# Optimization experiments

Hardware: AMD Instinct MI355X
Metric: run time of the kernel (lower is better)

## Reference

```python
import jax, jax.numpy as jnp
import numpy as np

N_EMBD = 1024
N_HEAD = 16
HEAD_DIM = N_EMBD // N_HEAD
B, T = 8, 1024


def setup_inputs() -> dict:
    key = jax.random.key(0)
    k1, k2, k3, k4 = jax.random.split(key, 4)
    x = jax.random.normal(k1, (B, T, N_EMBD), dtype=jnp.float32)
    # nn.Linear weight shapes: qkv (3C, C) no bias; proj (C, C) with bias
    w_qkv = jax.random.normal(k2, (3 * N_EMBD, N_EMBD), dtype=jnp.float32) * 0.02
    w_proj = jax.random.normal(k3, (N_EMBD, N_EMBD), dtype=jnp.float32) * 0.02
    b_proj = jax.random.normal(k4, (N_EMBD,), dtype=jnp.float32) * 0.02
    return {"x": x, "w_qkv": w_qkv, "w_proj": w_proj, "b_proj": b_proj}


def reference(x, w_qkv, w_proj, b_proj):
    Bq, Tq, C = x.shape
    qkv = jnp.einsum('btc,dc->btd', x, w_qkv)  # (B,T,3C)
    q, k, v = jnp.split(qkv, 3, axis=-1)
    def heads(t):
        return t.reshape(Bq, Tq, N_HEAD, HEAD_DIM).transpose(0, 2, 1, 3)  # (B,H,T,D)
    q, k, v = heads(q), heads(k), heads(v)
    scale = 1.0 / np.sqrt(HEAD_DIM).astype(np.float32)
    att = jnp.einsum('bhqd,bhkd->bhqk', q, k) * scale  # (B,H,T,T)
    causal = jnp.tril(jnp.ones((Tq, Tq), dtype=bool))
    att = jnp.where(causal, att, -jnp.inf)
    att = jax.nn.softmax(att, axis=-1)
    # dropout: eval mode -> identity
    y = jnp.einsum('bhqk,bhkd->bhqd', att, v)
    y = y.transpose(0, 2, 1, 3).reshape(Bq, Tq, C)
    return jnp.einsum('btc,dc->btd', y, w_proj) + b_proj
```

## Files before the change

### kernel.cpp

```cpp
#include <hip/hip_runtime.h>
#include <stdint.h>


#define Bn 8
#define Tn 1024
#define Cn 1024
#define Hn 16
#define Dn 64
#define Mn (Bn * Tn)
#define NQKV (3 * Cn)
#define QKS 2048

typedef unsigned short u16;
typedef float f32x4 __attribute__((ext_vector_type(4)));
typedef __bf16 bf16x8 __attribute__((ext_vector_type(8)));
typedef unsigned short ushx8 __attribute__((ext_vector_type(8)));
typedef unsigned short ushx4 __attribute__((ext_vector_type(4)));

__device__ __forceinline__ u16 f2bf(float f) {
  unsigned int u = __float_as_uint(f);
  u += 0x7fffu + ((u >> 16) & 1u);
  return (u16)(u >> 16);
}
__device__ __forceinline__ u16 f2bf_rna(float f) {
  return (u16)((__float_as_uint(f) + 0x8000u) >> 16);
}

__device__ __forceinline__ f32x4 mfma_bf16(ushx8 a, ushx8 b, f32x4 c) {
  return __builtin_amdgcn_mfma_f32_16x16x32_bf16(
      __builtin_bit_cast(bf16x8, a), __builtin_bit_cast(bf16x8, b), c, 0, 0, 0);
}

__device__ __forceinline__ void async16(const u16* g, u16* l) {
  __builtin_amdgcn_global_load_lds(
      (__attribute__((address_space(1))) void*)(void*)g,
      (__attribute__((address_space(3))) void*)l, 16, 0, 0);
}

template <int CTRL>
__device__ __forceinline__ float dppmov(float v) {
  return __builtin_bit_cast(float, __builtin_amdgcn_update_dpp(
      0, __builtin_bit_cast(int, v), CTRL, 0xf, 0xf, true));
}
__device__ __forceinline__ float red16max(float v) {
  v = fmaxf(v, dppmov<0xB1>(v));
  v = fmaxf(v, dppmov<0x4E>(v));
  v = fmaxf(v, dppmov<0x141>(v));
  v = fmaxf(v, dppmov<0x140>(v));
  return v;
}
__device__ __forceinline__ float red16sum(float v) {
  v += dppmov<0xB1>(v);
  v += dppmov<0x4E>(v);
  v += dppmov<0x141>(v);
  v += dppmov<0x140>(v);
  return v;
}

__global__ void cast3_kernel(const float* __restrict__ a, u16* __restrict__ oa, int na4,
                             const float* __restrict__ b, u16* __restrict__ ob, int nb4,
                             const float* __restrict__ c, u16* __restrict__ oc, int nc4) {
  int i = blockIdx.x * blockDim.x + threadIdx.x;
  const float* in;
  u16* out;
  if (i < na4) { in = a; out = oa; }
  else if (i < na4 + nb4) { in = b; out = ob; i -= na4; }
  else if (i < na4 + nb4 + nc4) { in = c; out = oc; i -= na4 + nb4; }
  else return;
  float4 v = ((const float4*)in)[i];
  ushx4 o = { f2bf(v.x), f2bf(v.y), f2bf(v.z), f2bf(v.w) };
  ((ushx4*)out)[i] = o;
}

#define SLOG2E 0.18033688011112042f
template <int QKV>
__global__ __launch_bounds__(256, 4) void gemm_bt(
    const u16* __restrict__ A, const u16* __restrict__ Bw,
    void* __restrict__ Cout, u16* __restrict__ vt,
    const float* __restrict__ bias, int N, int K) {
  __shared__ alignas(16) u16 As[128 * 32];
  __shared__ alignas(16) u16 Bs[128 * 32];

  const int tid = threadIdx.x;
  const int lane = tid & 63;
  const int wv = tid >> 6;
  const int quad = lane >> 4;
  const int l16 = lane & 15;
  const int m0 = blockIdx.x * 128;
  const int n0 = blockIdx.y * 128;
  const int wm = (wv >> 1) * 64;
  const int wn = (wv & 1) * 64;

  f32x4 acc[4][4];
#pragma unroll
  for (int i = 0; i < 4; ++i)
#pragma unroll
    for (int j = 0; j < 4; ++j) acc[i][j] = (f32x4){0.f, 0.f, 0.f, 0.f};

  const int r0 = tid >> 2;
  const int cc0 = tid & 3;
  const int gkc0 = cc0 ^ ((r0 >> 1) & 3);
  const int r1 = r0 + 64;
  const int gkc1 = cc0 ^ ((r1 >> 1) & 3);
  const u16* gA0 = A + (size_t)(m0 + r0) * K + gkc0 * 8;
  const u16* gA1 = A + (size_t)(m0 + r1) * K + gkc1 * 8;
  const u16* gB0 = Bw + (size_t)(n0 + r0) * K + gkc0 * 8;
  const u16* gB1 = Bw + (size_t)(n0 + r1) * K + gkc1 * 8;
  u16* lA0 = As + tid * 8;
  u16* lA1 = As + (256 + tid) * 8;
  u16* lB0 = Bs + tid * 8;
  u16* lB1 = Bs + (256 + tid) * 8;

  const u16* pa[4];
  const u16* pb[4];
#pragma unroll
  for (int mi = 0; mi < 4; ++mi) {
    int ra = wm + mi * 16 + l16;
    pa[mi] = As + ra * 32 + (quad ^ ((ra >> 1) & 3)) * 8;
    int rb = wn + mi * 16 + l16;
    pb[mi] = Bs + rb * 32 + (quad ^ ((rb >> 1) & 3)) * 8;
  }

  for (int k0 = 0; k0 < K; k0 += 32) {
    async16(gA0 + k0, lA0);
    async16(gA1 + k0, lA1);
    async16(gB0 + k0, lB0);
    async16(gB1 + k0, lB1);
    __syncthreads();
    ushx8 af[4], bf[4];
#pragma unroll
    for (int i = 0; i < 4; ++i) {
      af[i] = *(const ushx8*)pa[i];
      bf[i] = *(const ushx8*)pb[i];
    }
#pragma unroll
    for (int mi = 0; mi < 4; ++mi)
#pragma unroll
      for (int ni = 0; ni < 4; ++ni)
        acc[mi][ni] = mfma_bf16(af[mi], bf[ni], acc[mi][ni]);
    __syncthreads();
  }

  if constexpr (QKV) {
    if (n0 < 2 * Cn) {
#pragma unroll
      for (int mi = 0; mi < 4; ++mi) {
#pragma unroll
        for (int ni = 0; ni < 4; ++ni) {
          int col = n0 + wn + ni * 16 + l16;
          float sc = (col < Cn) ? SLOG2E : 1.f;
#pragma unroll
          for (int i = 0; i < 4; ++i) {
            int row = m0 + wm + mi * 16 + quad * 4 + i;
            ((u16*)Cout)[(size_t)row * QKS + col] = f2bf(acc[mi][ni][i] * sc);
          }
        }
      }
    } else {
#pragma unroll
      for (int mi = 0; mi < 4; ++mi) {
#pragma unroll
        for (int ni = 0; ni < 4; ++ni) {
          int colV = n0 + wn + ni * 16 + l16 - 2 * Cn;
          int hh = colV >> 6, dd = colV & 63;
          int row0 = m0 + wm + mi * 16 + quad * 4;
          int bb = row0 >> 10, tt = row0 & 1023;
          unsigned int lo = (unsigned int)f2bf(acc[mi][ni][0]) |
                            ((unsigned int)f2bf(acc[mi][ni][1]) << 16);
          unsigned int hi = (unsigned int)f2bf(acc[mi][ni][2]) |
                            ((unsigned int)f2bf(acc[mi][ni][3]) << 16);
          uint2 pk = {lo, hi};
          *(uint2*)&vt[((size_t)(bb * Hn + hh) * Dn + dd) * Tn + tt] = pk;
        }
      }
    }
  } else {
#pragma unroll
    for (int mi = 0; mi < 4; ++mi) {
#pragma unroll
      for (int ni = 0; ni < 4; ++ni) {
        int col = n0 + wn + ni * 16 + l16;
        float bv = bias[col];
#pragma unroll
        for (int i = 0; i < 4; ++i) {
          int row = m0 + wm + mi * 16 + quad * 4 + i;
          ((float*)Cout)[(size_t)row * N + col] = acc[mi][ni][i] + bv;
        }
      }
    }
  }
}

__global__ __launch_bounds__(256, 3) void attn_kernel(
    const u16* __restrict__ qk, const u16* __restrict__ vt,
    u16* __restrict__ out) {
  const int j = blockIdx.x, h = blockIdx.y, b = blockIdx.z;
  const int tid = threadIdx.x;
  const int lane = tid & 63;
  const int wv = tid >> 6;
  const int quad = lane >> 4;
  const int l16 = lane & 15;

  __shared__ alignas(16) u16 Ks[2][64 * 64];
  __shared__ alignas(16) u16 Vts[2][64 * 64];
  __shared__ alignas(16) u16 Ps[4][16 * 72];

  const u16* qb = qk + (size_t)b * Tn * QKS + h * Dn;
  const u16* kb = qk + (size_t)b * Tn * QKS + Cn + h * Dn;
  const u16* vtb = vt + (size_t)(b * Hn + h) * Dn * Tn;

  const int srow = tid >> 3;
  const int scc = tid & 7;
  u16* pswv = Ps[wv];

#pragma unroll 1
  for (int ph = 0; ph < 2; ++ph) {
    const int qt = ph ? (15 - j) : j;
    const int q0 = qt * 64;
    const int ntiles = qt + 1;

    ushx8 qf[2];
    {
      const u16* qp = qb + (size_t)(q0 + wv * 16 + l16) * QKS + quad * 8;
      qf[0] = *(const ushx8*)qp;
      qf[1] = *(const ushx8*)(qp + 32);
    }

    f32x4 o[4];
#pragma unroll
    for (int nt = 0; nt < 4; ++nt) o[nt] = (f32x4){0.f, 0.f, 0.f, 0.f};
    float mrow[4], lrow[4];
#pragma unroll
    for (int i = 0; i < 4; ++i) { mrow[i] = -__builtin_inff(); lrow[i] = 0.f; }

    __syncthreads();

#pragma unroll
    for (int c = 0; c < 2; ++c) {
      const int row = c * 32 + srow;
      const int gc = scc ^ (row & 7);
      async16(kb + (size_t)row * QKS + gc * 8, Ks[0] + (c * 256 + tid) * 8);
      async16(vtb + (size_t)row * Tn + gc * 8, Vts[0] + (c * 256 + tid) * 8);
    }

#pragma unroll 1
    for (int t = 0; t < ntiles; ++t) {
      const int kv0 = t * 64;
      const int bi = t & 1;
      __syncthreads();

      if (t + 1 < ntiles) {
        const int nkv0 = kv0 + 64;
        u16* kd = Ks[bi ^ 1];
        u16* vd = Vts[bi ^ 1];
#pragma unroll
        for (int c = 0; c < 2; ++c) {
          const int row = c * 32 + srow;
          const int gc = scc ^ (row & 7);
          async16(kb + (size_t)(nkv0 + row) * QKS + gc * 8, kd + (c * 256 + tid) * 8);
          async16(vtb + (size_t)row * Tn + nkv0 + gc * 8, vd + (c * 256 + tid) * 8);
        }
      }

      const u16* ks = Ks[bi];
      const u16* vs = Vts[bi];
      f32x4 s[4];
#pragma unroll
      for (int nt = 0; nt < 4; ++nt) s[nt] = (f32x4){0.f, 0.f, 0.f, 0.f};
#pragma unroll
      for (int nt = 0; nt < 4; ++nt) {
        const int rb = nt * 16 + l16;
        ushx8 b0 = *(const ushx8*)(ks + rb * 64 + (quad ^ (rb & 7)) * 8);
        ushx8 b1 = *(const ushx8*)(ks + rb * 64 + ((quad + 4) ^ (rb & 7)) * 8);
        s[nt] = mfma_bf16(qf[0], b0, s[nt]);
        s[nt] = mfma_bf16(qf[1], b1, s[nt]);
      }

      const bool dz = (kv0 + 64 > q0 + wv * 16);
#pragma unroll
      for (int i = 0; i < 4; ++i) {
        const int qr = q0 + wv * 16 + quad * 4 + i;
        float vv[4];
        float rmax = -__builtin_inff();
#pragma unroll
        for (int nt = 0; nt < 4; ++nt) {
          float v = s[nt][i];
          if (dz && (kv0 + nt * 16 + l16) > qr) v = -__builtin_inff();
          vv[nt] = v;
          rmax = fmaxf(rmax, v);
        }
        rmax = red16max(rmax);
        const float mnew = fmaxf(mrow[i], rmax);
        const float al = __builtin_amdgcn_exp2f(mrow[i] - mnew);
        mrow[i] = mnew;
        float rsum = 0.f;
#pragma unroll
        for (int nt = 0; nt < 4; ++nt) {
          float p = __builtin_amdgcn_exp2f(vv[nt] - mnew);
          rsum += p;
          pswv[(quad * 4 + i) * 72 + nt * 16 + l16] = f2bf_rna(p);
        }
        rsum = red16sum(rsum);
        lrow[i] = lrow[i] * al + rsum;
#pragma unroll
        for (int nt = 0; nt < 4; ++nt) o[nt][i] *= al;
      }

      ushx8 pf0, pf1;
      {
        const u16* pp = pswv + l16 * 72 + quad * 8;
        pf0 = *(const ushx8*)pp;
        pf1 = *(const ushx8*)(pp + 32);
      }

#pragma unroll
      for (int nt = 0; nt < 4; ++nt) {
        const int rb = nt * 16 + l16;
        ushx8 v0 = *(const ushx8*)(vs + rb * 64 + (quad ^ (rb & 7)) * 8);
        ushx8 v1 = *(const ushx8*)(vs + rb * 64 + ((quad + 4) ^ (rb & 7)) * 8);
        o[nt] = mfma_bf16(pf0, v0, o[nt]);
        o[nt] = mfma_bf16(pf1, v1, o[nt]);
      }
    }

#pragma unroll
    for (int i = 0; i < 4; ++i) {
      const float inv = 1.f / lrow[i];
      const int t = q0 + wv * 16 + quad * 4 + i;
      u16* op = out + ((size_t)(b * Tn + t)) * Cn + h * Dn + l16;
#pragma unroll
      for (int nt = 0; nt < 4; ++nt) op[nt * 16] = f2bf(o[nt][i] * inv);
    }
  }
}

extern "C" void kernel_launch(void* const* d_in, const int* in_sizes, int n_in,
                              void* d_out, int out_size, void* d_ws, size_t ws_size,
                              hipStream_t stream) {
  const float* x = (const float*)d_in[0];
  const float* w_qkv = (const float*)d_in[1];
  const float* w_proj = (const float*)d_in[2];
  const float* b_proj = (const float*)d_in[3];
  float* out = (float*)d_out;
  char* ws = (char*)d_ws;

  u16* xb     = (u16*)(ws);
  u16* wqkvb  = (u16*)(ws + 16777216);
  u16* wprojb = (u16*)(ws + 23068672);
  u16* qkb    = (u16*)(ws + 25165824);
  u16* vtb    = (u16*)(ws + 58720256);
  u16* yb     = (u16*)(ws + 75497472);

  cast3_kernel<<<12288, 256, 0, stream>>>(x, xb, 2097152,
                                          w_qkv, wqkvb, 786432,
                                          w_proj, wprojb, 262144);

  gemm_bt<1><<<dim3(Mn / 128, NQKV / 128), 256, 0, stream>>>(
      xb, wqkvb, (void*)qkb, vtb, nullptr, NQKV, Cn);

  attn_kernel<<<dim3(8, Hn, Bn), 256, 0, stream>>>(qkb, vtb, yb);

  gemm_bt<0><<<dim3(Mn / 128, Cn / 128), 256, 0, stream>>>(
      yb, wprojb, (void*)out, nullptr, b_proj, Cn, Cn);
}
```

Before: 244.2 us.

## Restructure GEMM to 128x256 tiles with double-buffered A and register-streamed B

The bf16 GEMM now computes a 128x256 output tile per block. Each wave owns a 64-column strip and all 128 rows. Only the A tile goes through LDS, now double-buffered with async copies so the next K-slice loads while the current one computes. B fragments are read directly from global memory into registers and prefetched one step ahead. This removes one barrier per K-step and all B shared-memory traffic, at the cost of more accumulator registers (occupancy hint lowered to 2), uncoalesced per-lane global B loads, and half as many blocks in the grid.

```diff
diff --git a/kernel.cpp b/kernel.cpp
--- a/kernel.cpp
+++ b/kernel.cpp
@@ -74,12 +74,11 @@
 
 #define SLOG2E 0.18033688011112042f
 template <int QKV>
-__global__ __launch_bounds__(256, 4) void gemm_bt(
+__global__ __launch_bounds__(256, 2) void gemm_bt(
     const u16* __restrict__ A, const u16* __restrict__ Bw,
     void* __restrict__ Cout, u16* __restrict__ vt,
     const float* __restrict__ bias, int N, int K) {
-  __shared__ alignas(16) u16 As[128 * 32];
-  __shared__ alignas(16) u16 Bs[128 * 32];
+  __shared__ alignas(16) u16 As[2][128 * 32];
 
   const int tid = threadIdx.x;
   const int lane = tid & 63;
@@ -87,13 +86,12 @@
   const int quad = lane >> 4;
   const int l16 = lane & 15;
   const int m0 = blockIdx.x * 128;
-  const int n0 = blockIdx.y * 128;
-  const int wm = (wv >> 1) * 64;
-  const int wn = (wv & 1) * 64;
-
-  f32x4 acc[4][4];
-#pragma unroll
-  for (int i = 0; i < 4; ++i)
+  const int n0 = blockIdx.y * 256;
+  const int wn = wv * 64;
+
+  f32x4 acc[8][4];
+#pragma unroll
+  for (int i = 0; i < 8; ++i)
 #pragma unroll
     for (int j = 0; j < 4; ++j) acc[i][j] = (f32x4){0.f, 0.f, 0.f, 0.f};
 
@@ -104,66 +102,80 @@
   const int gkc1 = cc0 ^ ((r1 >> 1) & 3);
   const u16* gA0 = A + (size_t)(m0 + r0) * K + gkc0 * 8;
   const u16* gA1 = A + (size_t)(m0 + r1) * K + gkc1 * 8;
-  const u16* gB0 = Bw + (size_t)(n0 + r0) * K + gkc0 * 8;
-  const u16* gB1 = Bw + (size_t)(n0 + r1) * K + gkc1 * 8;
-  u16* lA0 = As + tid * 8;
-  u16* lA1 = As + (256 + tid) * 8;
-  u16* lB0 = Bs + tid * 8;
-  u16* lB1 = Bs + (256 + tid) * 8;
-
-  const u16* pa[4];
-  const u16* pb[4];
-#pragma unroll
-  for (int mi = 0; mi < 4; ++mi) {
-    int ra = wm + mi * 16 + l16;
-    pa[mi] = As + ra * 32 + (quad ^ ((ra >> 1) & 3)) * 8;
-    int rb = wn + mi * 16 + l16;
-    pb[mi] = Bs + rb * 32 + (quad ^ ((rb >> 1) & 3)) * 8;
+
+  int aoff[8];
+#pragma unroll
+  for (int mi = 0; mi < 8; ++mi) {
+    int ra = mi * 16 + l16;
+    aoff[mi] = ra * 32 + (quad ^ ((ra >> 1) & 3)) * 8;
   }
 
-  for (int k0 = 0; k0 < K; k0 += 32) {
-    async16(gA0 + k0, lA0);
-    async16(gA1 + k0, lA1);
-    async16(gB0 + k0, lB0);
-    async16(gB1 + k0, lB1);
+  const u16* gB[4];
+#pragma unroll
+  for (int ni = 0; ni < 4; ++ni)
+    gB[ni] = Bw + (size_t)(n0 + wn + ni * 16 + l16) * K + quad * 8;
+
+  ushx8 bcur[4], bnxt[4];
+#pragma unroll
+  for (int ni = 0; ni < 4; ++ni) bcur[ni] = *(const ushx8*)gB[ni];
+
+  async16(gA0, As[0] + tid * 8);
+  async16(gA1, As[0] + (256 + tid) * 8);
+
+  const int nep = K >> 5;
+#pragma unroll 1
+  for (int e = 0; e < nep; ++e) {
+    const int k0 = e * 32;
     __syncthreads();
-    ushx8 af[4], bf[4];
-#pragma unroll
-    for (int i = 0; i < 4; ++i) {
-      af[i] = *(const ushx8*)pa[i];
-      bf[i] = *(const ushx8*)pb[i];
-    }
-#pragma unroll
-    for (int mi = 0; mi < 4; ++mi)
+
+    if (e + 1 < nep) {
+      u16* dst = As[(e + 1) & 1];
+      async16(gA0 + k0 + 32, dst + tid * 8);
+      async16(gA1 + k0 + 32, dst + (256 + tid) * 8);
 #pragma unroll
       for (int ni = 0; ni < 4; ++ni)
-        acc[mi][ni] = mfma_bf16(af[mi], bf[ni], acc[mi][ni]);
-    __syncthreads();
+        bnxt[ni] = *(const ushx8*)(gB[ni] + k0 + 32);
+    }
+
+    const u16* as = As[e & 1];
+    ushx8 af[8];
+#pragma unroll
+    for (int mi = 0; mi < 8; ++mi) af[mi] = *(const ushx8*)(as + aoff[mi]);
+#pragma unroll
+    for (int mi = 0; mi < 8; ++mi)
+#pragma unroll
+      for (int ni = 0; ni < 4; ++ni)
+        acc[mi][ni] = mfma_bf16(af[mi], bcur[ni], acc[mi][ni]);
+
+    if (e + 1 < nep) {
+#pragma unroll
+      for (int ni = 0; ni < 4; ++ni) bcur[ni] = bnxt[ni];
+    }
   }
 
   if constexpr (QKV) {
     if (n0 < 2 * Cn) {
-#pragma unroll
-      for (int mi = 0; mi < 4; ++mi) {
+      const float sc = (n0 < Cn) ? SLOG2E : 1.f;
+#pragma unroll
+      for (int mi = 0; mi < 8; ++mi) {
 #pragma unroll
         for (int ni = 0; ni < 4; ++ni) {
           int col = n0 + wn + ni * 16 + l16;
-          float sc = (col < Cn) ? SLOG2E : 1.f;
 #pragma unroll
           for (int i = 0; i < 4; ++i) {
-            int row = m0 + wm + mi * 16 + quad * 4 + i;
+            int row = m0 + mi * 16 + quad * 4 + i;
             ((u16*)Cout)[(size_t)row * QKS + col] = f2bf(acc[mi][ni][i] * sc);
           }
         }
       }
     } else {
 #pragma unroll
-      for (int mi = 0; mi < 4; ++mi) {
+      for (int mi = 0; mi < 8; ++mi) {
 #pragma unroll
         for (int ni = 0; ni < 4; ++ni) {
           int colV = n0 + wn + ni * 16 + l16 - 2 * Cn;
           int hh = colV >> 6, dd = colV & 63;
-          int row0 = m0 + wm + mi * 16 + quad * 4;
+          int row0 = m0 + mi * 16 + quad * 4;
           int bb = row0 >> 10, tt = row0 & 1023;
           unsigned int lo = (unsigned int)f2bf(acc[mi][ni][0]) |
                             ((unsigned int)f2bf(acc[mi][ni][1]) << 16);
@@ -176,14 +188,14 @@
     }
   } else {
 #pragma unroll
-    for (int mi = 0; mi < 4; ++mi) {
+    for (int mi = 0; mi < 8; ++mi) {
 #pragma unroll
       for (int ni = 0; ni < 4; ++ni) {
         int col = n0 + wn + ni * 16 + l16;
         float bv = bias[col];
 #pragma unroll
         for (int i = 0; i < 4; ++i) {
-          int row = m0 + wm + mi * 16 + quad * 4 + i;
+          int row = m0 + mi * 16 + quad * 4 + i;
           ((float*)Cout)[(size_t)row * N + col] = acc[mi][ni][i] + bv;
         }
       }
@@ -355,11 +367,11 @@
                                           w_qkv, wqkvb, 786432,
                                           w_proj, wprojb, 262144);
 
-  gemm_bt<1><<<dim3(Mn / 128, NQKV / 128), 256, 0, stream>>>(
+  gemm_bt<1><<<dim3(Mn / 128, NQKV / 256), 256, 0, stream>>>(
       xb, wqkvb, (void*)qkb, vtb, nullptr, NQKV, Cn);
 
   attn_kernel<<<dim3(8, Hn, Bn), 256, 0, stream>>>(qkb, vtb, yb);
 
-  gemm_bt<0><<<dim3(Mn / 128, Cn / 128), 256, 0, stream>>>(
+  gemm_bt<0><<<dim3(Mn / 128, Cn / 256), 256, 0, stream>>>(
       yb, wprojb, (void*)out, nullptr, b_proj, Cn, Cn);
 }
```

After: 260.9 us. 1.07x slower.

## Double-buffer LDS tiles in the GEMM kernel to overlap loads with MFMA

Applied to the files above, without the earlier changes.

Splits the GEMM shared-memory tiles into two buffers. The async global-to-LDS copy for the next K slice is issued while MFMAs run on the current slice, which drops one barrier per iteration and hides load latency. As a small side change, the per-column scale selection in the QKV epilogue is hoisted to a per-block constant. LDS use per block doubles, which could limit occupancy.

```diff
diff --git a/kernel.cpp b/kernel.cpp
--- a/kernel.cpp
+++ b/kernel.cpp
@@ -78,8 +78,8 @@
     const u16* __restrict__ A, const u16* __restrict__ Bw,
     void* __restrict__ Cout, u16* __restrict__ vt,
     const float* __restrict__ bias, int N, int K) {
-  __shared__ alignas(16) u16 As[128 * 32];
-  __shared__ alignas(16) u16 Bs[128 * 32];
+  __shared__ alignas(16) u16 As[2][128 * 32];
+  __shared__ alignas(16) u16 Bs[2][128 * 32];
 
   const int tid = threadIdx.x;
   const int lane = tid & 63;
@@ -106,49 +106,60 @@
   const u16* gA1 = A + (size_t)(m0 + r1) * K + gkc1 * 8;
   const u16* gB0 = Bw + (size_t)(n0 + r0) * K + gkc0 * 8;
   const u16* gB1 = Bw + (size_t)(n0 + r1) * K + gkc1 * 8;
-  u16* lA0 = As + tid * 8;
-  u16* lA1 = As + (256 + tid) * 8;
-  u16* lB0 = Bs + tid * 8;
-  u16* lB1 = Bs + (256 + tid) * 8;
-
-  const u16* pa[4];
-  const u16* pb[4];
+
+  int aoff[4], boff[4];
 #pragma unroll
   for (int mi = 0; mi < 4; ++mi) {
     int ra = wm + mi * 16 + l16;
-    pa[mi] = As + ra * 32 + (quad ^ ((ra >> 1) & 3)) * 8;
+    aoff[mi] = ra * 32 + (quad ^ ((ra >> 1) & 3)) * 8;
     int rb = wn + mi * 16 + l16;
-    pb[mi] = Bs + rb * 32 + (quad ^ ((rb >> 1) & 3)) * 8;
+    boff[mi] = rb * 32 + (quad ^ ((rb >> 1) & 3)) * 8;
   }
 
-  for (int k0 = 0; k0 < K; k0 += 32) {
-    async16(gA0 + k0, lA0);
-    async16(gA1 + k0, lA1);
-    async16(gB0 + k0, lB0);
-    async16(gB1 + k0, lB1);
+  async16(gA0, As[0] + tid * 8);
+  async16(gA1, As[0] + (256 + tid) * 8);
+  async16(gB0, Bs[0] + tid * 8);
+  async16(gB1, Bs[0] + (256 + tid) * 8);
+
+  const int nep = K >> 5;
+#pragma unroll 1
+  for (int e = 0; e < nep; ++e) {
+    const int bi = e & 1;
     __syncthreads();
+
+    if (e + 1 < nep) {
+      const int k1 = (e + 1) * 32;
+      u16* ad = As[bi ^ 1];
+      u16* bd = Bs[bi ^ 1];
+      async16(gA0 + k1, ad + tid * 8);
+      async16(gA1 + k1, ad + (256 + tid) * 8);
+      async16(gB0 + k1, bd + tid * 8);
+      async16(gB1 + k1, bd + (256 + tid) * 8);
+    }
+
+    const u16* as = As[bi];
+    const u16* bs = Bs[bi];
     ushx8 af[4], bf[4];
 #pragma unroll
     for (int i = 0; i < 4; ++i) {
-      af[i] = *(const ushx8*)pa[i];
-      bf[i] = *(const ushx8*)pb[i];
+      af[i] = *(const ushx8*)(as + aoff[i]);
+      bf[i] = *(const ushx8*)(bs + boff[i]);
     }
 #pragma unroll
     for (int mi = 0; mi < 4; ++mi)
 #pragma unroll
       for (int ni = 0; ni < 4; ++ni)
         acc[mi][ni] = mfma_bf16(af[mi], bf[ni], acc[mi][ni]);
-    __syncthreads();
   }
 
   if constexpr (QKV) {
     if (n0 < 2 * Cn) {
+      const float sc = (n0 < Cn) ? SLOG2E : 1.f;
 #pragma unroll
       for (int mi = 0; mi < 4; ++mi) {
 #pragma unroll
         for (int ni = 0; ni < 4; ++ni) {
           int col = n0 + wn + ni * 16 + l16;
-          float sc = (col < Cn) ? SLOG2E : 1.f;
 #pragma unroll
           for (int i = 0; i < 4; ++i) {
             int row = m0 + wm + mi * 16 + quad * 4 + i;
```

Measured after the change: 249.5 us. +2.2%, slower.

## Enlarge attention query tile to 128 rows with 8 waves and skip masked tiles

Applied to the files above, without the earlier changes.

The attention kernel now uses 512 threads (8 waves) per block covering a 128-row query tile, so each K/V tile loaded into shared memory is shared by twice as many query rows. The grid is halved to match, and each thread issues one async load per tile instead of two. Waves skip KV tiles that lie entirely above their diagonal. The causal mask is applied only on the diagonal tile, with a cheaper unmasked softmax path elsewhere. The per-tile row-sum reduction is deferred to a single reduction at the end. Risks include fewer blocks for load balancing, idle waves during skipped tiles, and register-pressure changes from the new launch bounds.

```diff
diff --git a/kernel.cpp b/kernel.cpp
--- a/kernel.cpp
+++ b/kernel.cpp
@@ -143,12 +143,12 @@
 
   if constexpr (QKV) {
     if (n0 < 2 * Cn) {
+      const float sc = (n0 < Cn) ? SLOG2E : 1.f;
 #pragma unroll
       for (int mi = 0; mi < 4; ++mi) {
 #pragma unroll
         for (int ni = 0; ni < 4; ++ni) {
           int col = n0 + wn + ni * 16 + l16;
-          float sc = (col < Cn) ? SLOG2E : 1.f;
 #pragma unroll
           for (int i = 0; i < 4; ++i) {
             int row = m0 + wm + mi * 16 + quad * 4 + i;
@@ -191,7 +191,7 @@
   }
 }
 
-__global__ __launch_bounds__(256, 3) void attn_kernel(
+__global__ __launch_bounds__(512, 4) void attn_kernel(
     const u16* __restrict__ qk, const u16* __restrict__ vt,
     u16* __restrict__ out) {
   const int j = blockIdx.x, h = blockIdx.y, b = blockIdx.z;
@@ -203,7 +203,7 @@
 
   __shared__ alignas(16) u16 Ks[2][64 * 64];
   __shared__ alignas(16) u16 Vts[2][64 * 64];
-  __shared__ alignas(16) u16 Ps[4][16 * 72];
+  __shared__ alignas(16) u16 Ps[8][16 * 72];
 
   const u16* qb = qk + (size_t)b * Tn * QKS + h * Dn;
   const u16* kb = qk + (size_t)b * Tn * QKS + Cn + h * Dn;
@@ -211,17 +211,19 @@
 
   const int srow = tid >> 3;
   const int scc = tid & 7;
+  const int sgc = scc ^ (srow & 7);
   u16* pswv = Ps[wv];
 
 #pragma unroll 1
   for (int ph = 0; ph < 2; ++ph) {
-    const int qt = ph ? (15 - j) : j;
-    const int q0 = qt * 64;
-    const int ntiles = qt + 1;
+    const int qt = ph ? (7 - j) : j;
+    const int q0w = qt * 128 + wv * 16;
+    const int ntiles = 2 * qt + 2;
+    const int tdiag = q0w >> 6;
 
     ushx8 qf[2];
     {
-      const u16* qp = qb + (size_t)(q0 + wv * 16 + l16) * QKS + quad * 8;
+      const u16* qp = qb + (size_t)(q0w + l16) * QKS + quad * 8;
       qf[0] = *(const ushx8*)qp;
       qf[1] = *(const ushx8*)(qp + 32);
     }
@@ -235,13 +237,8 @@
 
     __syncthreads();
 
-#pragma unroll
-    for (int c = 0; c < 2; ++c) {
-      const int row = c * 32 + srow;
-      const int gc = scc ^ (row & 7);
-      async16(kb + (size_t)row * QKS + gc * 8, Ks[0] + (c * 256 + tid) * 8);
-      async16(vtb + (size_t)row * Tn + gc * 8, Vts[0] + (c * 256 + tid) * 8);
-    }
+    async16(kb + (size_t)srow * QKS + sgc * 8, Ks[0] + tid * 8);
+    async16(vtb + (size_t)srow * Tn + sgc * 8, Vts[0] + tid * 8);
 
 #pragma unroll 1
     for (int t = 0; t < ntiles; ++t) {
@@ -251,16 +248,11 @@
 
       if (t + 1 < ntiles) {
         const int nkv0 = kv0 + 64;
-        u16* kd = Ks[bi ^ 1];
-        u16* vd = Vts[bi ^ 1];
-#pragma unroll
-        for (int c = 0; c < 2; ++c) {
-          const int row = c * 32 + srow;
-          const int gc = scc ^ (row & 7);
-          async16(kb + (size_t)(nkv0 + row) * QKS + gc * 8, kd + (c * 256 + tid) * 8);
-          async16(vtb + (size_t)row * Tn + nkv0 + gc * 8, vd + (c * 256 + tid) * 8);
-        }
-      }
+        async16(kb + (size_t)(nkv0 + srow) * QKS + sgc * 8, Ks[bi ^ 1] + tid * 8);
+        async16(vtb + (size_t)srow * Tn + nkv0 + sgc * 8, Vts[bi ^ 1] + tid * 8);
+      }
+
+      if (t > tdiag) continue;
 
       const u16* ks = Ks[bi];
       const u16* vs = Vts[bi];
@@ -276,34 +268,53 @@
         s[nt] = mfma_bf16(qf[1], b1, s[nt]);
       }
 
-      const bool dz = (kv0 + 64 > q0 + wv * 16);
-#pragma unroll
-      for (int i = 0; i < 4; ++i) {
-        const int qr = q0 + wv * 16 + quad * 4 + i;
-        float vv[4];
-        float rmax = -__builtin_inff();
-#pragma unroll
-        for (int nt = 0; nt < 4; ++nt) {
-          float v = s[nt][i];
-          if (dz && (kv0 + nt * 16 + l16) > qr) v = -__builtin_inff();
-          vv[nt] = v;
-          rmax = fmaxf(rmax, v);
-        }
-        rmax = red16max(rmax);
-        const float mnew = fmaxf(mrow[i], rmax);
-        const float al = __builtin_amdgcn_exp2f(mrow[i] - mnew);
-        mrow[i] = mnew;
-        float rsum = 0.f;
-#pragma unroll
-        for (int nt = 0; nt < 4; ++nt) {
-          float p = __builtin_amdgcn_exp2f(vv[nt] - mnew);
-          rsum += p;
-          pswv[(quad * 4 + i) * 72 + nt * 16 + l16] = f2bf_rna(p);
-        }
-        rsum = red16sum(rsum);
-        lrow[i] = lrow[i] * al + rsum;
-#pragma unroll
-        for (int nt = 0; nt < 4; ++nt) o[nt][i] *= al;
+      if (t == tdiag) {
+#pragma unroll
+        for (int i = 0; i < 4; ++i) {
+          const int qr = q0w + quad * 4 + i;
+          float vv[4];
+          float rmax = -__builtin_inff();
+#pragma unroll
+          for (int nt = 0; nt < 4; ++nt) {
+            float v = s[nt][i];
+            if ((kv0 + nt * 16 + l16) > qr) v = -__builtin_inff();
+            vv[nt] = v;
+            rmax = fmaxf(rmax, v);
+          }
+          rmax = red16max(rmax);
+          const float mnew = fmaxf(mrow[i], rmax);
+          const float al = __builtin_amdgcn_exp2f(mrow[i] - mnew);
+          mrow[i] = mnew;
+          float rsum = 0.f;
+#pragma unroll
+          for (int nt = 0; nt < 4; ++nt) {
+            float p = __builtin_amdgcn_exp2f(vv[nt] - mnew);
+            rsum += p;
+            pswv[(quad * 4 + i) * 72 + nt * 16 + l16] = f2bf_rna(p);
+          }
+          lrow[i] = lrow[i] * al + rsum;
+#pragma unroll
+          for (int nt = 0; nt < 4; ++nt) o[nt][i] *= al;
+        }
+      } else {
+#pragma unroll
+        for (int i = 0; i < 4; ++i) {
+          float rmax = fmaxf(fmaxf(s[0][i], s[1][i]), fmaxf(s[2][i], s[3][i]));
+          rmax = red16max(rmax);
+          const float mnew = fmaxf(mrow[i], rmax);
+          const float al = __builtin_amdgcn_exp2f(mrow[i] - mnew);
+          mrow[i] = mnew;
+          float rsum = 0.f;
+#pragma unroll
+          for (int nt = 0; nt < 4; ++nt) {
+            float p = __builtin_amdgcn_exp2f(s[nt][i] - mnew);
+            rsum += p;
+            pswv[(quad * 4 + i) * 72 + nt * 16 + l16] = f2bf_rna(p);
+          }
+          lrow[i] = lrow[i] * al + rsum;
+#pragma unroll
+          for (int nt = 0; nt < 4; ++nt) o[nt][i] *= al;
+        }
       }
 
       ushx8 pf0, pf1;
@@ -325,9 +336,9 @@
 
 #pragma unroll
     for (int i = 0; i < 4; ++i) {
-      const float inv = 1.f / lrow[i];
-      const int t = q0 + wv * 16 + quad * 4 + i;
-      u16* op = out + ((size_t)(b * Tn + t)) * Cn + h * Dn + l16;
+      const float inv = 1.f / red16sum(lrow[i]);
+      const int trow = q0w + quad * 4 + i;
+      u16* op = out + ((size_t)(b * Tn + trow)) * Cn + h * Dn + l16;
 #pragma unroll
       for (int nt = 0; nt < 4; ++nt) op[nt * 16] = f2bf(o[nt][i] * inv);
     }
@@ -358,7 +369,7 @@
   gemm_bt<1><<<dim3(Mn / 128, NQKV / 128), 256, 0, stream>>>(
       xb, wqkvb, (void*)qkb, vtb, nullptr, NQKV, Cn);
 
-  attn_kernel<<<dim3(8, Hn, Bn), 256, 0, stream>>>(qkb, vtb, yb);
+  attn_kernel<<<dim3(4, Hn, Bn), 512, 0, stream>>>(qkb, vtb, yb);
 
   gemm_bt<0><<<dim3(Mn / 128, Cn / 128), 256, 0, stream>>>(
       yb, wprojb, (void*)out, nullptr, b_proj, Cn, Cn);
```

Measured after the change: 229.5 us. 6.0% less time.
